# Optimization experiments

Measured on AMD Instinct MI355X. Metric: run time of the kernel, lower is better.

Reference implementation:

```python
import jax, jax.numpy as jnp
import numpy as np

S = 8          # num_syndromes (distance-3 surface code)
Q = 9          # num_qubits
F = 64         # n_node_features
H = 256        # hidden_size
ITERS = 3      # n_iters
B = 65536      # batch_size (shots)
N = B * S      # total nodes in batched graph
E = 2097152    # num edges (~avg degree 4)


def setup_inputs() -> dict:
    key = jax.random.key(0)
    ks = jax.random.split(key, 20)
    sc = 0.05
    inp = {
        "syndromes": jax.random.uniform(ks[0], (N, 1), dtype=jnp.float32),
        "edge_index": jax.random.randint(ks[1], (2, E), 0, N, dtype=jnp.int64),
        "batch_size": B,
        # embed: Linear(1, F)
        "embed_W": jax.random.normal(ks[2], (1, F), jnp.float32) * sc,
        "embed_b": jnp.zeros((F,), jnp.float32),
        # GCNConv per iter: weight (F,F) + bias (F,)
        "gcn_W": jax.random.normal(ks[3], (ITERS, F, F), jnp.float32) * sc,
        "gcn_b": jnp.zeros((ITERS, F), jnp.float32),
        # refine MLP per iter: F->H->F
        "ref_W1": jax.random.normal(ks[4], (ITERS, F, H), jnp.float32) * sc,
        "ref_b1": jnp.zeros((ITERS, H), jnp.float32),
        "ref_W2": jax.random.normal(ks[5], (ITERS, H, F), jnp.float32) * sc,
        "ref_b2": jnp.zeros((ITERS, F), jnp.float32),
        # error head per iter: F*S -> H -> H//2 -> Q
        "head_W1": jax.random.normal(ks[6], (ITERS, F * S, H), jnp.float32) * sc,
        "head_b1": jnp.zeros((ITERS, H), jnp.float32),
        "head_W2": jax.random.normal(ks[7], (ITERS, H, H // 2), jnp.float32) * sc,
        "head_b2": jnp.zeros((ITERS, H // 2), jnp.float32),
        "head_W3": jax.random.normal(ks[8], (ITERS, H // 2, Q), jnp.float32) * sc,
        "head_b3": jnp.zeros((ITERS, Q), jnp.float32),
    }
    return inp


def _gcn(x, src, dst, norm, W, b, n_nodes):
    # x' = D^{-1/2} (A+I) D^{-1/2} (x W) + b   (PyG GCNConv, eval mode)
    xw = x @ W                                  # [N, F]
    msg = xw[src] * norm[:, None]               # gather + edge-normalize
    out = jax.ops.segment_sum(msg, dst, num_segments=n_nodes)
    return out + b


def reference(syndromes, edge_index, batch_size,
              embed_W, embed_b, gcn_W, gcn_b,
              ref_W1, ref_b1, ref_W2, ref_b2,
              head_W1, head_b1, head_W2, head_b2, head_W3, head_b3):
    n_nodes = syndromes.shape[0]
    loops = jnp.arange(n_nodes, dtype=edge_index.dtype)
    src = jnp.concatenate([edge_index[0], loops])
    dst = jnp.concatenate([edge_index[1], loops])
    deg = jnp.zeros((n_nodes,), syndromes.dtype).at[dst].add(1.0)
    dinv = 1.0 / jnp.sqrt(deg)                  # deg >= 1 due to self-loops
    norm = dinv[src] * dinv[dst]

    h = syndromes @ embed_W + embed_b           # [N, F]
    outs = []
    for i in range(ITERS):
        h = _gcn(h, src, dst, norm, gcn_W[i], gcn_b[i], n_nodes)
        h = jax.nn.relu(h)
        r = jax.nn.relu(h @ ref_W1[i] + ref_b1[i]) @ ref_W2[i] + ref_b2[i]
        h = jax.nn.relu(h + r)
        h_all = h.reshape(batch_size, -1)        # [B, S*F]
        z = jax.nn.relu(h_all @ head_W1[i] + head_b1[i])
        z = jax.nn.relu(z @ head_W2[i] + head_b2[i])
        outs.append(jax.nn.sigmoid(z @ head_W3[i] + head_b3[i]))  # [B, Q]
    return tuple(outs)
```

## Files before the change

kernel.cpp:

```cpp
#include <hip/hip_runtime.h>
#include <cstdint>

#define NN 524288
#define NB 65536
#define NQ 9
#define NEDGE 2097152
#define NITERS 3

typedef __attribute__((ext_vector_type(8))) short bf16x8;
typedef __attribute__((ext_vector_type(4))) float f32x4;

__device__ __forceinline__ unsigned short f2b(float f) {
    union { float f; unsigned u; } v; v.f = f;
    unsigned u = v.u;
    u += 0x7FFFu + ((u >> 16) & 1u);
    return (unsigned short)(u >> 16);
}
__device__ __forceinline__ float b2f(unsigned short b) {
    union { unsigned u; float f; } v; v.u = ((unsigned)b) << 16;
    return v.f;
}
__device__ __forceinline__ float frelu(float v) { return v > 0.f ? v : 0.f; }

__device__ __forceinline__ int sw64(int r, int c)  { return r * 64  + (c ^ ((r & 7) << 3)); }


__global__ void k_cnt_init(int* __restrict__ cnt) {
    cnt[blockIdx.x * 256 + threadIdx.x] = 0;
}

__global__ void k_hist(const int* __restrict__ eidx, int* __restrict__ cnt) {
    int e = blockIdx.x * 256 + threadIdx.x;
    atomicAdd(&cnt[eidx[NEDGE + e]], 1);
}

__global__ void k_scan1(const int* __restrict__ cnt, int* __restrict__ rowptr,
                        int* __restrict__ bsum, float* __restrict__ dinv) {
    __shared__ int sd[256];
    int tid = threadIdx.x;
    int base = (blockIdx.x * 256 + tid) * 4;
    int c0 = cnt[base], c1 = cnt[base + 1], c2 = cnt[base + 2], c3 = cnt[base + 3];
    dinv[base]     = rsqrtf(1.f + (float)c0);
    dinv[base + 1] = rsqrtf(1.f + (float)c1);
    dinv[base + 2] = rsqrtf(1.f + (float)c2);
    dinv[base + 3] = rsqrtf(1.f + (float)c3);
    int t = c0 + c1 + c2 + c3;
    sd[tid] = t; __syncthreads();
    for (int o = 1; o < 256; o <<= 1) {
        int v = (tid >= o) ? sd[tid - o] : 0;
        __syncthreads();
        sd[tid] += v;
        __syncthreads();
    }
    int excl = sd[tid] - t;
    rowptr[base]     = excl;
    rowptr[base + 1] = excl + c0;
    rowptr[base + 2] = excl + c0 + c1;
    rowptr[base + 3] = excl + c0 + c1 + c2;
    if (tid == 255) bsum[blockIdx.x] = sd[255];
}

__global__ void k_scan2(int* __restrict__ bsum) {
    __shared__ int sd[512];
    int tid = threadIdx.x;
    int v = bsum[tid];
    sd[tid] = v; __syncthreads();
    for (int o = 1; o < 512; o <<= 1) {
        int u = (tid >= o) ? sd[tid - o] : 0;
        __syncthreads();
        sd[tid] += u;
        __syncthreads();
    }
    bsum[tid] = sd[tid] - v;
}

__global__ void k_scan3(int* __restrict__ rowptr, const int* __restrict__ bsum,
                        int* __restrict__ cursor) {
    int tid = threadIdx.x;
    int base = (blockIdx.x * 256 + tid) * 4;
    int off = bsum[blockIdx.x];
#pragma unroll
    for (int j = 0; j < 4; ++j) {
        int r = rowptr[base + j] + off;
        rowptr[base + j] = r;
        cursor[base + j] = r;
    }
    if (blockIdx.x == 511 && tid == 255) rowptr[NN] = NEDGE;
}

__global__ void k_fill(const int* __restrict__ eidx, int* __restrict__ cursor,
                       int* __restrict__ srcs) {
    int e = blockIdx.x * 256 + threadIdx.x;
    int s = eidx[e], d = eidx[NEDGE + e];
    int pos = atomicAdd(&cursor[d], 1);
    srcs[pos] = s;
}

__global__ void k_trans(const float* __restrict__ W, unsigned short* __restrict__ Wt,
                        int K, int M, int total) {
    int o = blockIdx.x * 256 + threadIdx.x;
    if (o >= total) return;
    int km = K * M;
    int it = o / km;
    int rem = o - it * km;
    int m = rem / K;
    int k = rem - m * K;
    Wt[o] = f2b(W[(size_t)it * km + (size_t)k * M + m]);
}



template<bool EMBED>
__global__ __launch_bounds__(256, 6) void k_gcnref(
    const int* __restrict__ rowptr, const int* __restrict__ srcs,
    const float* __restrict__ dinv,
    const float* __restrict__ syn, const float* __restrict__ embW,
    const float* __restrict__ embB,
    const unsigned short* __restrict__ hin,
    const unsigned short* __restrict__ Wgt, const float* __restrict__ bg,
    const unsigned short* __restrict__ W1t, const float* __restrict__ b1,
    const unsigned short* __restrict__ W2t, const float* __restrict__ b2,
    unsigned short* __restrict__ hout)
{
    __shared__ unsigned short tl[64 * 64];
    __shared__ unsigned short zl[64 * 64];
    const int tid = threadIdx.x, wid = tid >> 6, l = tid & 63;
    const int lr = l & 15, lkq = l >> 4;
    const int g = l >> 4, i = l & 15;
    const int rowBase = blockIdx.x * 64;
    const int nb = rowBase + wid * 16;

    float4 ew4, eb4;
    if (EMBED) {
        ew4 = *(const float4*)(embW + i * 4);
        eb4 = *(const float4*)(embB + i * 4);
    }

    for (int q = 0; q < 4; ++q) {
        const int node = nb + q * 4 + g;
        int beg = rowptr[node];
        int deg = rowptr[node + 1] - beg;
        int   sl = (i < deg) ? srcs[beg + i] : node;
        float wl = (i < deg) ? dinv[sl] : 0.f;

        float dn = dinv[node];
        float a0, a1, a2, a3;
        if (EMBED) {
            float s0 = syn[node];
            a0 = (s0 * ew4.x + eb4.x) * dn;
            a1 = (s0 * ew4.y + eb4.y) * dn;
            a2 = (s0 * ew4.z + eb4.z) * dn;
            a3 = (s0 * ew4.w + eb4.w) * dn;
        } else {
            ushort4 sv = *(const ushort4*)(hin + (size_t)node * 64 + i * 4);
            a0 = b2f(sv.x) * dn; a1 = b2f(sv.y) * dn;
            a2 = b2f(sv.z) * dn; a3 = b2f(sv.w) * dn;
        }

        int dmax = max(max(__shfl(deg, 0), __shfl(deg, 16)),
                       max(__shfl(deg, 32), __shfl(deg, 48)));
        int dfast = dmax < 16 ? dmax : 16;

        for (int p = 0; p < dfast; p += 8) {
            int   s[8]; float w[8];
#pragma unroll
            for (int u = 0; u < 8; ++u) {
                int idx = (l & 48) + p + u;
                s[u] = __shfl(sl, idx);
                w[u] = __shfl(wl, idx);
            }
            if (EMBED) {
                float sy[8];
#pragma unroll
                for (int u = 0; u < 8; ++u) sy[u] = syn[s[u]];
#pragma unroll
                for (int u = 0; u < 8; ++u) {
                    a0 += (sy[u] * ew4.x + eb4.x) * w[u];
                    a1 += (sy[u] * ew4.y + eb4.y) * w[u];
                    a2 += (sy[u] * ew4.z + eb4.z) * w[u];
                    a3 += (sy[u] * ew4.w + eb4.w) * w[u];
                }
            } else {
                ushort4 v[8];
#pragma unroll
                for (int u = 0; u < 8; ++u)
                    v[u] = *(const ushort4*)(hin + (size_t)s[u] * 64 + i * 4);
#pragma unroll
                for (int u = 0; u < 8; ++u) {
                    a0 += b2f(v[u].x) * w[u];
                    a1 += b2f(v[u].y) * w[u];
                    a2 += b2f(v[u].z) * w[u];
                    a3 += b2f(v[u].w) * w[u];
                }
            }
        }
        if (deg > 16) {
            for (int t = 16; t < deg; ++t) {
                int st = srcs[beg + t];
                float wt = dinv[st];
                if (EMBED) {
                    float sy = syn[st];
                    a0 += (sy * ew4.x + eb4.x) * wt;
                    a1 += (sy * ew4.y + eb4.y) * wt;
                    a2 += (sy * ew4.z + eb4.z) * wt;
                    a3 += (sy * ew4.w + eb4.w) * wt;
                } else {
                    ushort4 v = *(const ushort4*)(hin + (size_t)st * 64 + i * 4);
                    a0 += b2f(v.x) * wt; a1 += b2f(v.y) * wt;
                    a2 += b2f(v.z) * wt; a3 += b2f(v.w) * wt;
                }
            }
        }
        ushort4 o;
        o.x = f2b(a0 * dn); o.y = f2b(a1 * dn);
        o.z = f2b(a2 * dn); o.w = f2b(a3 * dn);
        *(ushort4*)&tl[sw64(wid * 16 + q * 4 + g, i * 4)] = o;
    }

    f32x4 ag[4];
#pragma unroll
    for (int mg = 0; mg < 4; ++mg) ag[mg] = (f32x4){0.f, 0.f, 0.f, 0.f};
#pragma unroll
    for (int kc = 0; kc < 64; kc += 32) {
        bf16x8 bfr = *(const bf16x8*)&tl[sw64(wid * 16 + lr, kc + lkq * 8)];
#pragma unroll
        for (int mg = 0; mg < 4; ++mg) {
            bf16x8 a = *(const bf16x8*)(Wgt + (size_t)(mg * 16 + lr) * 64 + kc + lkq * 8);
            ag[mg] = __builtin_amdgcn_mfma_f32_16x16x32_bf16(a, bfr, ag[mg], 0, 0, 0);
        }
    }
#pragma unroll
    for (int mg = 0; mg < 4; ++mg) {
        int m0 = mg * 16 + lkq * 4;
        float4 bb = *(const float4*)(bg + m0);
        ushort4 o;
        o.x = f2b(frelu(ag[mg][0] + bb.x));
        o.y = f2b(frelu(ag[mg][1] + bb.y));
        o.z = f2b(frelu(ag[mg][2] + bb.z));
        o.w = f2b(frelu(ag[mg][3] + bb.w));
        *(ushort4*)&tl[sw64(wid * 16 + lr, m0)] = o;
    }
    __syncthreads();

    f32x4 r2[4];
#pragma unroll
    for (int mg = 0; mg < 4; ++mg) r2[mg] = (f32x4){0.f, 0.f, 0.f, 0.f};

#pragma unroll
    for (int qt = 0; qt < 4; ++qt) {
        f32x4 z1a[4];
#pragma unroll
        for (int ng = 0; ng < 4; ++ng) z1a[ng] = (f32x4){0.f, 0.f, 0.f, 0.f};
#pragma unroll
        for (int kc = 0; kc < 64; kc += 32) {
            bf16x8 a = *(const bf16x8*)(W1t +
                (size_t)(qt * 64 + wid * 16 + lr) * 64 + kc + lkq * 8);
#pragma unroll
            for (int ng = 0; ng < 4; ++ng) {
                bf16x8 bfr = *(const bf16x8*)&tl[sw64(ng * 16 + lr, kc + lkq * 8)];
                z1a[ng] = __builtin_amdgcn_mfma_f32_16x16x32_bf16(a, bfr, z1a[ng], 0, 0, 0);
            }
        }
        {
            int m0 = wid * 16 + lkq * 4;
            float4 bb = *(const float4*)(b1 + qt * 64 + m0);
#pragma unroll
            for (int ng = 0; ng < 4; ++ng) {
                int n = ng * 16 + lr;
                ushort4 o;
                o.x = f2b(frelu(z1a[ng][0] + bb.x));
                o.y = f2b(frelu(z1a[ng][1] + bb.y));
                o.z = f2b(frelu(z1a[ng][2] + bb.z));
                o.w = f2b(frelu(z1a[ng][3] + bb.w));
                *(ushort4*)&zl[sw64(n, m0)] = o;
            }
        }
        __syncthreads();

#pragma unroll
        for (int kc = 0; kc < 64; kc += 32) {
            bf16x8 bz = *(const bf16x8*)&zl[sw64(wid * 16 + lr, kc + lkq * 8)];
#pragma unroll
            for (int mg = 0; mg < 4; ++mg) {
                bf16x8 a = *(const bf16x8*)(W2t +
                    (size_t)(mg * 16 + lr) * 256 + qt * 64 + kc + lkq * 8);
                r2[mg] = __builtin_amdgcn_mfma_f32_16x16x32_bf16(a, bz, r2[mg], 0, 0, 0);
            }
        }
        if (qt < 3) __syncthreads();
    }

    {
        int n = wid * 16 + lr;
#pragma unroll
        for (int mg = 0; mg < 4; ++mg) {
            int m0 = mg * 16 + lkq * 4;
            float4 bb = *(const float4*)(b2 + m0);
            ushort4 rs = *(const ushort4*)&tl[sw64(n, m0)];
            ushort4 o;
            o.x = f2b(frelu(r2[mg][0] + bb.x + b2f(rs.x)));
            o.y = f2b(frelu(r2[mg][1] + bb.y + b2f(rs.y)));
            o.z = f2b(frelu(r2[mg][2] + bb.z + b2f(rs.z)));
            o.w = f2b(frelu(r2[mg][3] + bb.w + b2f(rs.w)));
            *(ushort4*)&tl[sw64(n, m0)] = o;
        }
    }
    __syncthreads();
    {
        int r = tid >> 2, c16 = (tid & 3) * 16;
        bf16x8 v0 = *(const bf16x8*)&tl[sw64(r, c16)];
        bf16x8 v1 = *(const bf16x8*)&tl[sw64(r, c16 + 8)];
        *(bf16x8*)(hout + (size_t)(rowBase + r) * 64 + c16) = v0;
        *(bf16x8*)(hout + (size_t)(rowBase + r) * 64 + c16 + 8) = v1;
    }
}

__global__ __launch_bounds__(256) void k_head(const unsigned short* __restrict__ hb,
                                              const unsigned short* __restrict__ W1t,
                                              const float* __restrict__ b1,
                                              const unsigned short* __restrict__ W2t,
                                              const float* __restrict__ b2,
                                              const unsigned short* __restrict__ W3t,
                                              const float* __restrict__ b3,
                                              float* __restrict__ out) {
    __shared__ unsigned short z1[64][280];
    __shared__ unsigned short z2[64][152];
    const int tid = threadIdx.x, wid = tid >> 6, l = tid & 63;
    const int lr = l & 15, lkq = l >> 4;
    const unsigned short* hall = hb + (size_t)blockIdx.x * 64 * 512;

    f32x4 acc1[4][4];
#pragma unroll
    for (int mg = 0; mg < 4; ++mg)
#pragma unroll
        for (int ng = 0; ng < 4; ++ng) acc1[mg][ng] = (f32x4){0.f, 0.f, 0.f, 0.f};

    for (int kc = 0; kc < 512; kc += 32) {
        bf16x8 bfr[4];
#pragma unroll
        for (int ng = 0; ng < 4; ++ng)
            bfr[ng] = *(const bf16x8*)(hall + (size_t)(ng * 16 + lr) * 512 + kc + lkq * 8);
#pragma unroll
        for (int mg = 0; mg < 4; ++mg) {
            bf16x8 a = *(const bf16x8*)(W1t + (size_t)(wid * 64 + mg * 16 + lr) * 512 + kc + lkq * 8);
#pragma unroll
            for (int ng = 0; ng < 4; ++ng)
                acc1[mg][ng] = __builtin_amdgcn_mfma_f32_16x16x32_bf16(a, bfr[ng], acc1[mg][ng], 0, 0, 0);
        }
    }
#pragma unroll
    for (int mg = 0; mg < 4; ++mg) {
        int m0 = wid * 64 + mg * 16 + lkq * 4;
        float4 bb = *(const float4*)(b1 + m0);
#pragma unroll
        for (int ng = 0; ng < 4; ++ng) {
            int n = ng * 16 + lr;
            ushort4 o;
            o.x = f2b(frelu(acc1[mg][ng][0] + bb.x));
            o.y = f2b(frelu(acc1[mg][ng][1] + bb.y));
            o.z = f2b(frelu(acc1[mg][ng][2] + bb.z));
            o.w = f2b(frelu(acc1[mg][ng][3] + bb.w));
            *(ushort4*)&z1[n][m0] = o;
        }
    }
    __syncthreads();

    f32x4 acc2[2][4];
#pragma unroll
    for (int mg = 0; mg < 2; ++mg)
#pragma unroll
        for (int ng = 0; ng < 4; ++ng) acc2[mg][ng] = (f32x4){0.f, 0.f, 0.f, 0.f};
#pragma unroll
    for (int kc = 0; kc < 256; kc += 32) {
        bf16x8 bfr[4];
#pragma unroll
        for (int ng = 0; ng < 4; ++ng)
            bfr[ng] = *(const bf16x8*)&z1[ng * 16 + lr][kc + lkq * 8];
#pragma unroll
        for (int mg = 0; mg < 2; ++mg) {
            bf16x8 a = *(const bf16x8*)(W2t + (size_t)(wid * 32 + mg * 16 + lr) * 256 + kc + lkq * 8);
#pragma unroll
            for (int ng = 0; ng < 4; ++ng)
                acc2[mg][ng] = __builtin_amdgcn_mfma_f32_16x16x32_bf16(a, bfr[ng], acc2[mg][ng], 0, 0, 0);
        }
    }
#pragma unroll
    for (int mg = 0; mg < 2; ++mg) {
        int m0 = wid * 32 + mg * 16 + lkq * 4;
        float4 bb = *(const float4*)(b2 + m0);
#pragma unroll
        for (int ng = 0; ng < 4; ++ng) {
            int n = ng * 16 + lr;
            ushort4 o;
            o.x = f2b(frelu(acc2[mg][ng][0] + bb.x));
            o.y = f2b(frelu(acc2[mg][ng][1] + bb.y));
            o.z = f2b(frelu(acc2[mg][ng][2] + bb.z));
            o.w = f2b(frelu(acc2[mg][ng][3] + bb.w));
            *(ushort4*)&z2[n][m0] = o;
        }
    }
    __syncthreads();

    f32x4 acc3 = (f32x4){0.f, 0.f, 0.f, 0.f};
    int arow = lr < 9 ? lr : 8;
#pragma unroll
    for (int kc = 0; kc < 128; kc += 32) {
        bf16x8 bz = *(const bf16x8*)&z2[wid * 16 + lr][kc + lkq * 8];
        bf16x8 a = *(const bf16x8*)(W3t + (size_t)arow * 128 + kc + lkq * 8);
        acc3 = __builtin_amdgcn_mfma_f32_16x16x32_bf16(a, bz, acc3, 0, 0, 0);
    }
    {
        long shot = (long)blockIdx.x * 64 + wid * 16 + lr;
#pragma unroll
        for (int r = 0; r < 4; ++r) {
            int m = lkq * 4 + r;
            if (m < 9) {
                float v = acc3[r] + b3[m];
                out[shot * 9 + m] = 1.f / (1.f + expf(-v));
            }
        }
    }
}


extern "C" void kernel_launch(void* const* d_in, const int* in_sizes, int n_in,
                              void* d_out, int out_size, void* d_ws, size_t ws_size,
                              hipStream_t stream) {
    const float* syn  = (const float*)d_in[0];
    const int*   eidx = (const int*)d_in[1];
    const float* embW = (const float*)d_in[3];
    const float* embB = (const float*)d_in[4];
    const float* gcnW = (const float*)d_in[5];
    const float* gcnB = (const float*)d_in[6];
    const float* rW1  = (const float*)d_in[7];
    const float* rB1  = (const float*)d_in[8];
    const float* rW2  = (const float*)d_in[9];
    const float* rB2  = (const float*)d_in[10];
    const float* hW1  = (const float*)d_in[11];
    const float* hB1  = (const float*)d_in[12];
    const float* hW2  = (const float*)d_in[13];
    const float* hB2  = (const float*)d_in[14];
    const float* hW3  = (const float*)d_in[15];
    const float* hB3  = (const float*)d_in[16];
    float* out = (float*)d_out;

    unsigned short* h0     = (unsigned short*)d_ws;
    unsigned short* h1     = h0 + (size_t)NN * 64;
    int*            srcs   = (int*)(h1 + (size_t)NN * 64);
    int*            rowptr = srcs + NEDGE;
    int*            cnt    = rowptr + NN + 256;
    int*            bsum   = cnt + NN;
    float*          dinv   = (float*)(bsum + 512);
    unsigned short* gcnWt  = (unsigned short*)(dinv + NN);
    unsigned short* rW1t   = gcnWt + 3 * 64 * 64;
    unsigned short* rW2t   = rW1t + 3 * 64 * 256;
    unsigned short* hW1t   = rW2t + 3 * 256 * 64;
    unsigned short* hW2t   = hW1t + 3 * 512 * 256;
    unsigned short* hW3t   = hW2t + 3 * 256 * 128;

    k_trans<<<(3*64*64   + 255)/256, 256, 0, stream>>>(gcnW, gcnWt, 64, 64,  3*64*64);
    k_trans<<<(3*64*256  + 255)/256, 256, 0, stream>>>(rW1,  rW1t,  64, 256, 3*64*256);
    k_trans<<<(3*256*64  + 255)/256, 256, 0, stream>>>(rW2,  rW2t,  256, 64, 3*256*64);
    k_trans<<<(3*512*256 + 255)/256, 256, 0, stream>>>(hW1,  hW1t,  512, 256, 3*512*256);
    k_trans<<<(3*256*128 + 255)/256, 256, 0, stream>>>(hW2,  hW2t,  256, 128, 3*256*128);
    k_trans<<<(3*128*9   + 255)/256, 256, 0, stream>>>(hW3,  hW3t,  128, 9,   3*128*9);

    k_cnt_init<<<NN / 256, 256, 0, stream>>>(cnt);
    k_hist<<<NEDGE / 256, 256, 0, stream>>>(eidx, cnt);
    k_scan1<<<512, 256, 0, stream>>>(cnt, rowptr, bsum, dinv);
    k_scan2<<<1, 512, 0, stream>>>(bsum);
    k_scan3<<<512, 256, 0, stream>>>(rowptr, bsum, cnt);
    k_fill<<<NEDGE / 256, 256, 0, stream>>>(eidx, cnt, srcs);

    unsigned short* hcur = h0;
    unsigned short* hnxt = h1;
    for (int i = 0; i < NITERS; ++i) {
        unsigned short* hdst = (i == 0) ? h0 : hnxt;
        if (i == 0) {
            k_gcnref<true><<<NN / 64, 256, 0, stream>>>(
                rowptr, srcs, dinv, syn, embW, embB, nullptr,
                gcnWt, gcnB,
                rW1t, rB1, rW2t, rB2, h0);
        } else {
            k_gcnref<false><<<NN / 64, 256, 0, stream>>>(
                rowptr, srcs, dinv, nullptr, nullptr, nullptr, hcur,
                gcnWt + (size_t)i * 64 * 64, gcnB + (size_t)i * 64,
                rW1t + (size_t)i * 64 * 256, rB1 + (size_t)i * 256,
                rW2t + (size_t)i * 256 * 64, rB2 + (size_t)i * 64, hdst);
        }
        k_head<<<NB / 64, 256, 0, stream>>>(hdst,
                                            hW1t + (size_t)i * 512 * 256, hB1 + (size_t)i * 256,
                                            hW2t + (size_t)i * 256 * 128, hB2 + (size_t)i * 128,
                                            hW3t + (size_t)i * 128 * 9,   hB3 + (size_t)i * 9,
                                            out + (size_t)i * NB * NQ);
        if (i == 0) { hcur = h0; hnxt = h1; }
        else { unsigned short* t = hcur; hcur = hdst; hnxt = t; }
    }
}
```

Before: 1.217 ms.

## Fuse head of iteration i into GCN kernel of iteration i+1 and restructure head MLP

Merges each iteration's error-head work into the next iteration's GCN+refine launch by interleaving one head block every nine blocks, so both read the same h buffer in a single launch and the head's tail latency overlaps with GCN work. The head kernel is reorganised to compute its first layer in 64-column quarters that feed straight into the second layer. This cuts LDS to 12K shorts, with a swizzled layout and fewer live accumulators, allowing more resident blocks. The embed launch raises its occupancy hint to 8, and a standalone head kernel remains for the last iteration. The cost is heterogeneous blocks within one launch, which can unbalance the work and increase register pressure.

```diff
diff --git a/kernel.cpp b/kernel.cpp
--- a/kernel.cpp
+++ b/kernel.cpp
@@ -23,6 +23,7 @@
 __device__ __forceinline__ float frelu(float v) { return v > 0.f ? v : 0.f; }
 
 __device__ __forceinline__ int sw64(int r, int c)  { return r * 64  + (c ^ ((r & 7) << 3)); }
+__device__ __forceinline__ int sw128(int r, int c) { return r * 128 + (c ^ ((r & 7) << 3)); }
 
 
 __global__ void k_cnt_init(int* __restrict__ cnt) {
@@ -109,9 +110,105 @@
 }
 
 
-
-template<bool EMBED>
-__global__ __launch_bounds__(256, 6) void k_gcnref(
+__device__ __forceinline__ void head_block(
+    int t, unsigned short* smem,
+    const unsigned short* __restrict__ hb,
+    const unsigned short* __restrict__ W1t, const float* __restrict__ b1,
+    const unsigned short* __restrict__ W2t, const float* __restrict__ b2,
+    const unsigned short* __restrict__ W3t, const float* __restrict__ b3,
+    float* __restrict__ out)
+{
+    unsigned short* z1q = smem;
+    unsigned short* z2  = smem + 4096;
+    const int tid = threadIdx.x, wid = tid >> 6, l = tid & 63;
+    const int lr = l & 15, lkq = l >> 4;
+    const unsigned short* hall = hb + (size_t)t * 64 * 512;
+
+    f32x4 acc2[2][4];
+#pragma unroll
+    for (int mg = 0; mg < 2; ++mg)
+#pragma unroll
+        for (int ng = 0; ng < 4; ++ng) acc2[mg][ng] = (f32x4){0.f, 0.f, 0.f, 0.f};
+
+#pragma unroll
+    for (int qt = 0; qt < 4; ++qt) {
+        f32x4 a1[4];
+#pragma unroll
+        for (int ng = 0; ng < 4; ++ng) a1[ng] = (f32x4){0.f, 0.f, 0.f, 0.f};
+        for (int kc = 0; kc < 512; kc += 32) {
+            bf16x8 a = *(const bf16x8*)(W1t + (size_t)(qt * 64 + wid * 16 + lr) * 512 + kc + lkq * 8);
+#pragma unroll
+            for (int ng = 0; ng < 4; ++ng) {
+                bf16x8 bfr = *(const bf16x8*)(hall + (size_t)(ng * 16 + lr) * 512 + kc + lkq * 8);
+                a1[ng] = __builtin_amdgcn_mfma_f32_16x16x32_bf16(a, bfr, a1[ng], 0, 0, 0);
+            }
+        }
+        if (qt) __syncthreads();
+        {
+            int m0 = wid * 16 + lkq * 4;
+            float4 bb = *(const float4*)(b1 + qt * 64 + m0);
+#pragma unroll
+            for (int ng = 0; ng < 4; ++ng) {
+                int n = ng * 16 + lr;
+                ushort4 o;
+                o.x = f2b(frelu(a1[ng][0] + bb.x));
+                o.y = f2b(frelu(a1[ng][1] + bb.y));
+                o.z = f2b(frelu(a1[ng][2] + bb.z));
+                o.w = f2b(frelu(a1[ng][3] + bb.w));
+                *(ushort4*)&z1q[sw64(n, m0)] = o;
+            }
+        }
+        __syncthreads();
+#pragma unroll
+        for (int kc = 0; kc < 64; kc += 32) {
+#pragma unroll
+            for (int mg = 0; mg < 2; ++mg) {
+                bf16x8 a = *(const bf16x8*)(W2t + (size_t)(wid * 32 + mg * 16 + lr) * 256 + qt * 64 + kc + lkq * 8);
+#pragma unroll
+                for (int ng = 0; ng < 4; ++ng) {
+                    bf16x8 bz = *(const bf16x8*)&z1q[sw64(ng * 16 + lr, kc + lkq * 8)];
+                    acc2[mg][ng] = __builtin_amdgcn_mfma_f32_16x16x32_bf16(a, bz, acc2[mg][ng], 0, 0, 0);
+                }
+            }
+        }
+    }
+#pragma unroll
+    for (int mg = 0; mg < 2; ++mg) {
+        int m0 = wid * 32 + mg * 16 + lkq * 4;
+        float4 bb = *(const float4*)(b2 + m0);
+#pragma unroll
+        for (int ng = 0; ng < 4; ++ng) {
+            int n = ng * 16 + lr;
+            ushort4 o;
+            o.x = f2b(frelu(acc2[mg][ng][0] + bb.x));
+            o.y = f2b(frelu(acc2[mg][ng][1] + bb.y));
+            o.z = f2b(frelu(acc2[mg][ng][2] + bb.z));
+            o.w = f2b(frelu(acc2[mg][ng][3] + bb.w));
+            *(ushort4*)&z2[sw128(n, m0)] = o;
+        }
+    }
+    __syncthreads();
+    f32x4 a3 = (f32x4){0.f, 0.f, 0.f, 0.f};
+    int arow = lr < 9 ? lr : 8;
+#pragma unroll
+    for (int kc = 0; kc < 128; kc += 32) {
+        bf16x8 bz = *(const bf16x8*)&z2[sw128(wid * 16 + lr, kc + lkq * 8)];
+        bf16x8 a = *(const bf16x8*)(W3t + (size_t)arow * 128 + kc + lkq * 8);
+        a3 = __builtin_amdgcn_mfma_f32_16x16x32_bf16(a, bz, a3, 0, 0, 0);
+    }
+    {
+        long shot = (long)t * 64 + wid * 16 + lr;
+#pragma unroll
+        for (int r = 0; r < 4; ++r) {
+            int m = lkq * 4 + r;
+            if (m < 9) out[shot * 9 + m] = 1.f / (1.f + expf(-(a3[r] + b3[m])));
+        }
+    }
+}
+
+
+template<bool EMBED, bool HASHEAD, int MINW>
+__global__ __launch_bounds__(256, MINW) void k_gcnref(
     const int* __restrict__ rowptr, const int* __restrict__ srcs,
     const float* __restrict__ dinv,
     const float* __restrict__ syn, const float* __restrict__ embW,
@@ -120,14 +217,29 @@
     const unsigned short* __restrict__ Wgt, const float* __restrict__ bg,
     const unsigned short* __restrict__ W1t, const float* __restrict__ b1,
     const unsigned short* __restrict__ W2t, const float* __restrict__ b2,
-    unsigned short* __restrict__ hout)
+    unsigned short* __restrict__ hout,
+    const unsigned short* __restrict__ hW1t, const float* __restrict__ hb1,
+    const unsigned short* __restrict__ hW2t, const float* __restrict__ hb2,
+    const unsigned short* __restrict__ hW3t, const float* __restrict__ hb3,
+    float* __restrict__ headOut)
 {
-    __shared__ unsigned short tl[64 * 64];
-    __shared__ unsigned short zl[64 * 64];
+    __shared__ unsigned short smem[HASHEAD ? 12288 : 8192];
+
+    int blk = blockIdx.x;
+    if (HASHEAD) {
+        if (blk % 9 == 4) {
+            head_block(blk / 9, smem, hin, hW1t, hb1, hW2t, hb2, hW3t, hb3, headOut);
+            return;
+        }
+        blk = blk - blk / 9 - ((blk % 9) > 4 ? 1 : 0);
+    }
+
+    unsigned short* tl = smem;
+    unsigned short* zl = smem + 4096;
     const int tid = threadIdx.x, wid = tid >> 6, l = tid & 63;
     const int lr = l & 15, lkq = l >> 4;
     const int g = l >> 4, i = l & 15;
-    const int rowBase = blockIdx.x * 64;
+    const int rowBase = blk * 64;
     const int nb = rowBase + wid * 16;
 
     float4 ew4, eb4;
@@ -315,111 +427,15 @@
     }
 }
 
-__global__ __launch_bounds__(256) void k_head(const unsigned short* __restrict__ hb,
-                                              const unsigned short* __restrict__ W1t,
-                                              const float* __restrict__ b1,
-                                              const unsigned short* __restrict__ W2t,
-                                              const float* __restrict__ b2,
-                                              const unsigned short* __restrict__ W3t,
-                                              const float* __restrict__ b3,
-                                              float* __restrict__ out) {
-    __shared__ unsigned short z1[64][280];
-    __shared__ unsigned short z2[64][152];
-    const int tid = threadIdx.x, wid = tid >> 6, l = tid & 63;
-    const int lr = l & 15, lkq = l >> 4;
-    const unsigned short* hall = hb + (size_t)blockIdx.x * 64 * 512;
-
-    f32x4 acc1[4][4];
-#pragma unroll
-    for (int mg = 0; mg < 4; ++mg)
-#pragma unroll
-        for (int ng = 0; ng < 4; ++ng) acc1[mg][ng] = (f32x4){0.f, 0.f, 0.f, 0.f};
-
-    for (int kc = 0; kc < 512; kc += 32) {
-        bf16x8 bfr[4];
-#pragma unroll
-        for (int ng = 0; ng < 4; ++ng)
-            bfr[ng] = *(const bf16x8*)(hall + (size_t)(ng * 16 + lr) * 512 + kc + lkq * 8);
-#pragma unroll
-        for (int mg = 0; mg < 4; ++mg) {
-            bf16x8 a = *(const bf16x8*)(W1t + (size_t)(wid * 64 + mg * 16 + lr) * 512 + kc + lkq * 8);
-#pragma unroll
-            for (int ng = 0; ng < 4; ++ng)
-                acc1[mg][ng] = __builtin_amdgcn_mfma_f32_16x16x32_bf16(a, bfr[ng], acc1[mg][ng], 0, 0, 0);
-        }
-    }
-#pragma unroll
-    for (int mg = 0; mg < 4; ++mg) {
-        int m0 = wid * 64 + mg * 16 + lkq * 4;
-        float4 bb = *(const float4*)(b1 + m0);
-#pragma unroll
-        for (int ng = 0; ng < 4; ++ng) {
-            int n = ng * 16 + lr;
-            ushort4 o;
-            o.x = f2b(frelu(acc1[mg][ng][0] + bb.x));
-            o.y = f2b(frelu(acc1[mg][ng][1] + bb.y));
-            o.z = f2b(frelu(acc1[mg][ng][2] + bb.z));
-            o.w = f2b(frelu(acc1[mg][ng][3] + bb.w));
-            *(ushort4*)&z1[n][m0] = o;
-        }
-    }
-    __syncthreads();
-
-    f32x4 acc2[2][4];
-#pragma unroll
-    for (int mg = 0; mg < 2; ++mg)
-#pragma unroll
-        for (int ng = 0; ng < 4; ++ng) acc2[mg][ng] = (f32x4){0.f, 0.f, 0.f, 0.f};
-#pragma unroll
-    for (int kc = 0; kc < 256; kc += 32) {
-        bf16x8 bfr[4];
-#pragma unroll
-        for (int ng = 0; ng < 4; ++ng)
-            bfr[ng] = *(const bf16x8*)&z1[ng * 16 + lr][kc + lkq * 8];
-#pragma unroll
-        for (int mg = 0; mg < 2; ++mg) {
-            bf16x8 a = *(const bf16x8*)(W2t + (size_t)(wid * 32 + mg * 16 + lr) * 256 + kc + lkq * 8);
-#pragma unroll
-            for (int ng = 0; ng < 4; ++ng)
-                acc2[mg][ng] = __builtin_amdgcn_mfma_f32_16x16x32_bf16(a, bfr[ng], acc2[mg][ng], 0, 0, 0);
-        }
-    }
-#pragma unroll
-    for (int mg = 0; mg < 2; ++mg) {
-        int m0 = wid * 32 + mg * 16 + lkq * 4;
-        float4 bb = *(const float4*)(b2 + m0);
-#pragma unroll
-        for (int ng = 0; ng < 4; ++ng) {
-            int n = ng * 16 + lr;
-            ushort4 o;
-            o.x = f2b(frelu(acc2[mg][ng][0] + bb.x));
-            o.y = f2b(frelu(acc2[mg][ng][1] + bb.y));
-            o.z = f2b(frelu(acc2[mg][ng][2] + bb.z));
-            o.w = f2b(frelu(acc2[mg][ng][3] + bb.w));
-            *(ushort4*)&z2[n][m0] = o;
-        }
-    }
-    __syncthreads();
-
-    f32x4 acc3 = (f32x4){0.f, 0.f, 0.f, 0.f};
-    int arow = lr < 9 ? lr : 8;
-#pragma unroll
-    for (int kc = 0; kc < 128; kc += 32) {
-        bf16x8 bz = *(const bf16x8*)&z2[wid * 16 + lr][kc + lkq * 8];
-        bf16x8 a = *(const bf16x8*)(W3t + (size_t)arow * 128 + kc + lkq * 8);
-        acc3 = __builtin_amdgcn_mfma_f32_16x16x32_bf16(a, bz, acc3, 0, 0, 0);
-    }
-    {
-        long shot = (long)blockIdx.x * 64 + wid * 16 + lr;
-#pragma unroll
-        for (int r = 0; r < 4; ++r) {
-            int m = lkq * 4 + r;
-            if (m < 9) {
-                float v = acc3[r] + b3[m];
-                out[shot * 9 + m] = 1.f / (1.f + expf(-v));
-            }
-        }
-    }
+__global__ __launch_bounds__(256, 6) void k_headq(
+    const unsigned short* __restrict__ hb,
+    const unsigned short* __restrict__ W1t, const float* __restrict__ b1,
+    const unsigned short* __restrict__ W2t, const float* __restrict__ b2,
+    const unsigned short* __restrict__ W3t, const float* __restrict__ b3,
+    float* __restrict__ out)
+{
+    __shared__ unsigned short smem[12288];
+    head_block(blockIdx.x, smem, hb, W1t, b1, W2t, b2, W3t, b3, out);
 }
 
 
@@ -472,28 +488,32 @@
     k_scan3<<<512, 256, 0, stream>>>(rowptr, bsum, cnt);
     k_fill<<<NEDGE / 256, 256, 0, stream>>>(eidx, cnt, srcs);
 
-    unsigned short* hcur = h0;
-    unsigned short* hnxt = h1;
-    for (int i = 0; i < NITERS; ++i) {
-        unsigned short* hdst = (i == 0) ? h0 : hnxt;
-        if (i == 0) {
-            k_gcnref<true><<<NN / 64, 256, 0, stream>>>(
-                rowptr, srcs, dinv, syn, embW, embB, nullptr,
-                gcnWt, gcnB,
-                rW1t, rB1, rW2t, rB2, h0);
-        } else {
-            k_gcnref<false><<<NN / 64, 256, 0, stream>>>(
-                rowptr, srcs, dinv, nullptr, nullptr, nullptr, hcur,
-                gcnWt + (size_t)i * 64 * 64, gcnB + (size_t)i * 64,
-                rW1t + (size_t)i * 64 * 256, rB1 + (size_t)i * 256,
-                rW2t + (size_t)i * 256 * 64, rB2 + (size_t)i * 64, hdst);
-        }
-        k_head<<<NB / 64, 256, 0, stream>>>(hdst,
-                                            hW1t + (size_t)i * 512 * 256, hB1 + (size_t)i * 256,
-                                            hW2t + (size_t)i * 256 * 128, hB2 + (size_t)i * 128,
-                                            hW3t + (size_t)i * 128 * 9,   hB3 + (size_t)i * 9,
-                                            out + (size_t)i * NB * NQ);
-        if (i == 0) { hcur = h0; hnxt = h1; }
-        else { unsigned short* t = hcur; hcur = hdst; hnxt = t; }
-    }
-}
+    k_gcnref<true, false, 8><<<NN / 64, 256, 0, stream>>>(
+        rowptr, srcs, dinv, syn, embW, embB, nullptr,
+        gcnWt, gcnB, rW1t, rB1, rW2t, rB2, h0,
+        nullptr, nullptr, nullptr, nullptr, nullptr, nullptr, nullptr);
+
+    k_gcnref<false, true, 6><<<NN / 64 + NB / 64, 256, 0, stream>>>(
+        rowptr, srcs, dinv, nullptr, nullptr, nullptr, h0,
+        gcnWt + (size_t)1 * 64 * 64, gcnB + 64,
+        rW1t + (size_t)1 * 64 * 256, rB1 + 256,
+        rW2t + (size_t)1 * 256 * 64, rB2 + 64, h1,
+        hW1t, hB1, hW2t, hB2, hW3t, hB3, out);
+
+    k_gcnref<false, true, 6><<<NN / 64 + NB / 64, 256, 0, stream>>>(
+        rowptr, srcs, dinv, nullptr, nullptr, nullptr, h1,
+        gcnWt + (size_t)2 * 64 * 64, gcnB + 2 * 64,
+        rW1t + (size_t)2 * 64 * 256, rB1 + 2 * 256,
+        rW2t + (size_t)2 * 256 * 64, rB2 + 2 * 64, h0,
+        hW1t + (size_t)1 * 512 * 256, hB1 + 256,
+        hW2t + (size_t)1 * 256 * 128, hB2 + 128,
+        hW3t + (size_t)1 * 128 * 9,   hB3 + 9,
+        out + (size_t)NB * NQ);
+
+    k_headq<<<NB / 64, 256, 0, stream>>>(
+        h0,
+        hW1t + (size_t)2 * 512 * 256, hB1 + 2 * 256,
+        hW2t + (size_t)2 * 256 * 128, hB2 + 2 * 128,
+        hW3t + (size_t)2 * 128 * 9,   hB3 + 2 * 9,
+        out + (size_t)2 * NB * NQ);
+}
```

New measurement: 1.713 ms. 1.41x slower.
